# Performance work log

Measured on AMD Instinct MI355X. Metric: run time of the kernel, lower is better.

Reference implementation:

```python
import jax, jax.numpy as jnp
import numpy as np

SCALES = (8, 16, 32)
RATIOS = (0.5, 1.0, 2.0)
STRIDE = 16
K = len(SCALES) * len(RATIOS)
PRE_NMS = 6000
POST_NMS = 2000
NMS_THRESH = 0.7
ROIS_PER_IMG = 128
FG_ROIS = 32
FG_THRESH = 0.5
BG_HI = 0.5
BG_LO = 0.1
NUM_GT = 20
BBOX_CLIP = 4.135  # log(1000/16), standard delta clamp


def _generate_anchors(image_width, image_height):
    base = float(STRIDE)
    ctr = (base - 1.0) / 2.0
    size = base * base
    ratios = np.array(RATIOS, dtype=np.float64)
    scales = np.array(SCALES, dtype=np.float64)
    ws = np.round(np.sqrt(size / ratios))
    hs = np.round(ws * ratios)
    ws = (ws[:, None] * scales[None, :]).reshape(-1)  # (K,) ratio-major
    hs = (hs[:, None] * scales[None, :]).reshape(-1)
    anchors = np.stack([ctr - 0.5 * (ws - 1), ctr - 0.5 * (hs - 1),
                        ctr + 0.5 * (ws - 1), ctr + 0.5 * (hs - 1)], axis=1)  # (K,4)
    fw = image_width // STRIDE
    fh = image_height // STRIDE
    sx = np.arange(fw) * STRIDE
    sy = np.arange(fh) * STRIDE
    sxx, syy = np.meshgrid(sx, sy)  # (fh, fw)
    shifts = np.stack([sxx.ravel(), syy.ravel(), sxx.ravel(), syy.ravel()], axis=1)  # (fh*fw,4)
    all_anchors = (shifts[:, None, :] + anchors[None, :, :]).reshape(-1, 4)  # (fh*fw*K,4), K fastest
    return jnp.asarray(all_anchors, jnp.float32)


def _conv2d(x, w, b):
    y = jax.lax.conv_general_dilated(x, w, (1, 1), 'SAME',
                                     dimension_numbers=('NHWC', 'HWIO', 'NHWC'))
    return y + b


def _bbox_transform_inv(anchors, deltas):
    w = anchors[:, 2] - anchors[:, 0] + 1.0
    h = anchors[:, 3] - anchors[:, 1] + 1.0
    cx = anchors[:, 0] + 0.5 * w
    cy = anchors[:, 1] + 0.5 * h
    dx, dy = deltas[:, 0], deltas[:, 1]
    dw = jnp.clip(deltas[:, 2], -BBOX_CLIP, BBOX_CLIP)
    dh = jnp.clip(deltas[:, 3], -BBOX_CLIP, BBOX_CLIP)
    pcx = dx * w + cx
    pcy = dy * h + cy
    pw = jnp.exp(dw) * w
    ph = jnp.exp(dh) * h
    return jnp.stack([pcx - 0.5 * pw, pcy - 0.5 * ph,
                      pcx + 0.5 * pw, pcy + 0.5 * ph], axis=1)


def _pairwise_iou(a, b):
    area_a = (a[:, 2] - a[:, 0] + 1.0) * (a[:, 3] - a[:, 1] + 1.0)
    area_b = (b[:, 2] - b[:, 0] + 1.0) * (b[:, 3] - b[:, 1] + 1.0)
    xx1 = jnp.maximum(a[:, None, 0], b[None, :, 0])
    yy1 = jnp.maximum(a[:, None, 1], b[None, :, 1])
    xx2 = jnp.minimum(a[:, None, 2], b[None, :, 2])
    yy2 = jnp.minimum(a[:, None, 3], b[None, :, 3])
    iw = jnp.clip(xx2 - xx1 + 1.0, 0.0)
    ih = jnp.clip(yy2 - yy1 + 1.0, 0.0)
    inter = iw * ih
    return inter / (area_a[:, None] + area_b[None, :] - inter)


def _nms_keep(boxes, thresh):
    # boxes assumed sorted by score descending; greedy suppression
    n = boxes.shape[0]
    iou = _pairwise_iou(boxes, boxes)  # (n, n)
    idx = jnp.arange(n)
    def body(i, keep):
        sup = (iou[i] > thresh) & (idx > i)
        return jnp.where(keep[i], keep & ~sup, keep)
    return jax.lax.fori_loop(0, n, body, jnp.ones((n,), jnp.bool_))


def _forward(inputs, w_shared, b_shared, w_cls, b_cls, w_bbox, b_bbox,
             gt_boxes, image_width, image_height):
    fh = image_height // STRIDE
    fw = image_width // STRIDE
    anchors = _generate_anchors(image_width, image_height)  # (fh*fw*K, 4)

    shared = _conv2d(inputs, w_shared, b_shared)
    rpn_cls_score = _conv2d(shared, w_cls, b_cls)      # (1, fh, fw, 2K)
    rpn_bbox_pred = _conv2d(shared, w_bbox, b_bbox)    # (1, fh, fw, 4K)

    # softmax over the 2 (bg, fg) channels per anchor
    cls_prob = jax.nn.softmax(rpn_cls_score.reshape(1, fh, fw, K, 2), axis=-1)
    fg_scores = cls_prob[..., 1].reshape(-1)           # (fh*fw*K,)
    deltas = rpn_bbox_pred.reshape(-1, 4)              # (fh*fw*K, 4)

    # ---- proposal_layer ----
    proposals = _bbox_transform_inv(anchors, deltas)
    proposals = jnp.stack([
        jnp.clip(proposals[:, 0], 0.0, image_width - 1.0),
        jnp.clip(proposals[:, 1], 0.0, image_height - 1.0),
        jnp.clip(proposals[:, 2], 0.0, image_width - 1.0),
        jnp.clip(proposals[:, 3], 0.0, image_height - 1.0)], axis=1)

    top_scores, order = jax.lax.top_k(fg_scores, PRE_NMS)
    top_boxes = proposals[order]                       # (PRE_NMS, 4), score-sorted

    keep = _nms_keep(jax.lax.stop_gradient(top_boxes), NMS_THRESH)
    n = PRE_NMS
    rank = jnp.where(keep, jnp.arange(n), n + jnp.arange(n))
    sel = jnp.argsort(rank)[:POST_NMS]                 # kept boxes first, score order
    roi_boxes = top_boxes[sel]                         # (POST_NMS, 4)
    roi_scores = top_scores[sel]
    rois = jnp.concatenate([jnp.zeros((POST_NMS, 1), roi_boxes.dtype), roi_boxes], axis=1)

    # ---- proposal_target_layer (deterministic top-k sampling) ----
    ov = _pairwise_iou(roi_boxes, gt_boxes[:, :4])     # (POST_NMS, NUM_GT)
    max_ov = ov.max(axis=1)
    fg_key = jnp.where(max_ov >= FG_THRESH, max_ov, -1.0)
    _, fg_idx = jax.lax.top_k(fg_key, FG_ROIS)
    bg_key = jnp.where((max_ov < BG_HI) & (max_ov >= BG_LO), max_ov, -1.0)
    _, bg_idx = jax.lax.top_k(bg_key, ROIS_PER_IMG - FG_ROIS)
    keep_inds = jnp.concatenate([fg_idx, bg_idx])      # (128,)
    return rois[keep_inds]                             # (128, 5)


def setup_inputs() -> dict:
    key = jax.random.key(0)
    ks = jax.random.split(key, 10)
    C_in, C_mid = 1024, 256
    inputs = jax.random.normal(ks[0], (1, 64, 64, C_in), jnp.float32)
    w_shared = jax.random.normal(ks[1], (3, 3, C_in, C_mid), jnp.float32) * np.sqrt(2.0 / (9 * C_in))
    b_shared = jnp.zeros((C_mid,), jnp.float32)
    w_cls = jax.random.normal(ks[2], (1, 1, C_mid, 2 * K), jnp.float32) * np.sqrt(2.0 / C_mid)
    b_cls = jnp.zeros((2 * K,), jnp.float32)
    w_bbox = jax.random.normal(ks[3], (1, 1, C_mid, 4 * K), jnp.float32) * (0.1 * np.sqrt(2.0 / C_mid))
    b_bbox = jnp.zeros((4 * K,), jnp.float32)
    # valid gt boxes inside a 1024x1024 image
    cx = jax.random.uniform(ks[4], (NUM_GT,), minval=100.0, maxval=900.0)
    cy = jax.random.uniform(ks[5], (NUM_GT,), minval=100.0, maxval=900.0)
    bw = jax.random.uniform(ks[6], (NUM_GT,), minval=32.0, maxval=300.0)
    bh = jax.random.uniform(ks[7], (NUM_GT,), minval=32.0, maxval=300.0)
    cls = jax.random.randint(ks[8], (NUM_GT,), 1, 21).astype(jnp.float32)
    gt_boxes = jnp.stack([jnp.clip(cx - bw / 2, 0.0, 1023.0), jnp.clip(cy - bh / 2, 0.0, 1023.0),
                          jnp.clip(cx + bw / 2, 0.0, 1023.0), jnp.clip(cy + bh / 2, 0.0, 1023.0),
                          cls], axis=1)
    return {"inputs": inputs, "w_shared": w_shared, "b_shared": b_shared,
            "w_cls": w_cls, "b_cls": b_cls, "w_bbox": w_bbox, "b_bbox": b_bbox,
            "gt_boxes": gt_boxes, "image_width": 1024, "image_height": 1024}


def reference(inputs, w_shared, b_shared, w_cls, b_cls, w_bbox, b_bbox,
              gt_boxes, image_width, image_height):
    return _forward(inputs, w_shared, b_shared, w_cls, b_cls, w_bbox, b_bbox,
                    gt_boxes, image_width, image_height)
```

## Files before the change

### kernel.cpp

```cpp
#include <hip/hip_runtime.h>
#include <cstdint>
#include <cstddef>

#define M_POS 4096
#define NCH   256
#define KTOT  9216
#define NANCH 36864
#define NSORT 65536
#define PRE   6000
#define POST  2000
#define NGRP  94
#define MROW  6016
#define NSLOT 14

typedef unsigned long long u64;
typedef unsigned int u32;

__device__ __forceinline__ u32 ord_f32(float f) {
  u32 u = __float_as_uint(f);
  return (u & 0x80000000u) ? ~u : (u | 0x80000000u);
}

__global__ __launch_bounds__(256) void conv3x3(const float* __restrict__ in,
                                               const float* __restrict__ wgt,
                                               float* __restrict__ part,
                                               int kPer) {
  __shared__ __align__(16) float As[16][128];
  __shared__ __align__(16) float Bs[16][128];
  int tid = threadIdx.x;
  int bm = blockIdx.x << 7;
  int bn = blockIdx.y << 7;
  int kBeg = blockIdx.z * kPer;
  int am = tid & 127;
  int aq = (tid >> 7) << 2;
  int gm = bm + am;
  int y = gm >> 6, x = gm & 63;
  int bkk = tid >> 5;
  int bn4 = (tid & 31) << 2;
  int ty = tid >> 4, tx = tid & 15;

  float acc[8][8];
#pragma unroll
  for (int i = 0; i < 8; ++i)
#pragma unroll
    for (int j = 0; j < 8; ++j) acc[i][j] = 0.f;

  for (int k0 = kBeg; k0 < kBeg + kPer; k0 += 16) {
#pragma unroll
    for (int p = 0; p < 2; ++p) {
      int kk = aq + (p << 3);
      int k = k0 + kk;
      int tap = k >> 10;
      int c = k & 1023;
      int iy = y + tap / 3 - 1;
      int ix = x + tap % 3 - 1;
      float4 v = make_float4(0.f, 0.f, 0.f, 0.f);
      if (iy >= 0 && iy < 64 && ix >= 0 && ix < 64)
        v = *(const float4*)(in + (size_t)((((iy << 6) + ix) << 10) + c));
      As[kk + 0][am] = v.x;
      As[kk + 1][am] = v.y;
      As[kk + 2][am] = v.z;
      As[kk + 3][am] = v.w;
    }
#pragma unroll
    for (int p = 0; p < 2; ++p) {
      int kk = bkk + (p << 3);
      *(float4*)&Bs[kk][bn4] =
          *(const float4*)(wgt + (size_t)(k0 + kk) * NCH + bn + bn4);
    }
    __syncthreads();
#pragma unroll
    for (int kk = 0; kk < 16; ++kk) {
      float4 a0 = *(const float4*)&As[kk][ty << 2];
      float4 a1 = *(const float4*)&As[kk][64 + (ty << 2)];
      float4 b0 = *(const float4*)&Bs[kk][tx << 2];
      float4 b1 = *(const float4*)&Bs[kk][64 + (tx << 2)];
      float a[8] = {a0.x, a0.y, a0.z, a0.w, a1.x, a1.y, a1.z, a1.w};
      float b[8] = {b0.x, b0.y, b0.z, b0.w, b1.x, b1.y, b1.z, b1.w};
#pragma unroll
      for (int i = 0; i < 8; ++i)
#pragma unroll
        for (int j = 0; j < 8; ++j) acc[i][j] += a[i] * b[j];
    }
    __syncthreads();
  }
  size_t ob = (size_t)blockIdx.z * ((size_t)M_POS * NCH);
#pragma unroll
  for (int i = 0; i < 8; ++i) {
    int row = bm + ((i < 4) ? ((ty << 2) + i) : (64 + (ty << 2) + i - 4));
    float4 o0 = make_float4(acc[i][0], acc[i][1], acc[i][2], acc[i][3]);
    float4 o1 = make_float4(acc[i][4], acc[i][5], acc[i][6], acc[i][7]);
    *(float4*)(part + ob + (size_t)row * NCH + bn + (tx << 2)) = o0;
    *(float4*)(part + ob + (size_t)row * NCH + bn + 64 + (tx << 2)) = o1;
  }
}

__global__ __launch_bounds__(256) void reduce_bias(const float* __restrict__ part,
                                                   const float* __restrict__ bias,
                                                   float* __restrict__ outp, int ks) {
  int idx = blockIdx.x * 256 + threadIdx.x;
  float v = 0.f;
  for (int s = 0; s < ks; ++s) v += part[(size_t)s * (M_POS * NCH) + idx];
  outp[idx] = v + bias[idx & 255];
}

__global__ __launch_bounds__(64) void conv1x1(const float* __restrict__ sh,
                                              const float* __restrict__ wc,
                                              const float* __restrict__ bc,
                                              const float* __restrict__ wb,
                                              const float* __restrict__ bb2,
                                              float* __restrict__ cls,
                                              float* __restrict__ bbox) {
  __shared__ float row[256];
  int pos = blockIdx.x;
  int tid = threadIdx.x;
  *(float4*)&row[tid * 4] = *(const float4*)(sh + (size_t)pos * 256 + tid * 4);
  __syncthreads();
  if (tid < 18) {
    float acc = bc[tid];
    for (int c = 0; c < 256; ++c) acc += row[c] * wc[c * 18 + tid];
    cls[(size_t)pos * 18 + tid] = acc;
  } else if (tid < 54) {
    int n = tid - 18;
    float acc = bb2[n];
    for (int c = 0; c < 256; ++c) acc += row[c] * wb[c * 36 + n];
    bbox[(size_t)pos * 36 + n] = acc;
  }
}

__global__ __launch_bounds__(256) void proposals_k(const float* __restrict__ cls,
                                                   const float* __restrict__ bb,
                                                   float* __restrict__ scores,
                                                   float* __restrict__ prop) {
  int idx = blockIdx.x * 256 + threadIdx.x;
  if (idx >= NANCH) return;
  int a = idx % 9;
  int pos = idx / 9;
  int x = pos & 63, y = pos >> 6;
  float s0 = cls[(size_t)pos * 18 + 2 * a];
  float s1 = cls[(size_t)pos * 18 + 2 * a + 1];
  float mx = fmaxf(s0, s1);
  float e0 = expf(s0 - mx), e1 = expf(s1 - mx);
  scores[idx] = e1 / (e0 + e1);
  const float AW[9] = {184.f, 368.f, 736.f, 128.f, 256.f, 512.f, 88.f, 176.f, 352.f};
  const float AH[9] = {96.f, 192.f, 384.f, 128.f, 256.f, 512.f, 176.f, 352.f, 704.f};
  float w = AW[a], h = AH[a];
  float cx = (float)(x * 16) + 8.0f;
  float cy = (float)(y * 16) + 8.0f;
  float dx = bb[(size_t)pos * 36 + 4 * a + 0];
  float dy = bb[(size_t)pos * 36 + 4 * a + 1];
  float dw = bb[(size_t)pos * 36 + 4 * a + 2];
  float dh = bb[(size_t)pos * 36 + 4 * a + 3];
  dw = fminf(fmaxf(dw, -4.135f), 4.135f);
  dh = fminf(fmaxf(dh, -4.135f), 4.135f);
  float pcx = dx * w + cx;
  float pcy = dy * h + cy;
  float pw = expf(dw) * w;
  float ph = expf(dh) * h;
  float x1 = pcx - 0.5f * pw, y1 = pcy - 0.5f * ph;
  float x2 = pcx + 0.5f * pw, y2 = pcy + 0.5f * ph;
  x1 = fminf(fmaxf(x1, 0.f), 1023.f);
  y1 = fminf(fmaxf(y1, 0.f), 1023.f);
  x2 = fminf(fmaxf(x2, 0.f), 1023.f);
  y2 = fminf(fmaxf(y2, 0.f), 1023.f);
  prop[(size_t)idx * 4 + 0] = x1;
  prop[(size_t)idx * 4 + 1] = y1;
  prop[(size_t)idx * 4 + 2] = x2;
  prop[(size_t)idx * 4 + 3] = y2;
}

__global__ __launch_bounds__(256) void build_keys(const float* __restrict__ scores,
                                                  u64* __restrict__ keys) {
  int i = blockIdx.x * 256 + threadIdx.x;
  if (i >= NSORT) return;
  u64 k = 0ull;
  if (i < NANCH) {
    u32 u = ord_f32(scores[i]);
    k = ((u64)u << 32) | (u64)(0xFFFFFFFFu - (u32)i);
  }
  keys[i] = k;
}

__global__ __launch_bounds__(1024) void sort_local(u64* keys) {
  __shared__ u64 s[2048];
  int base = blockIdx.x * 2048;
  s[threadIdx.x] = keys[base + threadIdx.x];
  s[threadIdx.x + 1024] = keys[base + threadIdx.x + 1024];
  __syncthreads();
  for (int k = 2; k <= 2048; k <<= 1) {
    for (int j = k >> 1; j >= 1; j >>= 1) {
      int t = threadIdx.x;
      int i = ((t & ~(j - 1)) << 1) | (t & (j - 1));
      int p = i | j;
      bool desc = (((base + i) & k) == 0);
      u64 a = s[i], b = s[p];
      if (desc ? (a < b) : (a > b)) { s[i] = b; s[p] = a; }
      __syncthreads();
    }
  }
  keys[base + threadIdx.x] = s[threadIdx.x];
  keys[base + threadIdx.x + 1024] = s[threadIdx.x + 1024];
}

__device__ __forceinline__ void cmpswap(u64& a, u64& b, bool desc) {
  if (desc ? (a < b) : (a > b)) { u64 t = a; a = b; b = t; }
}

__global__ __launch_bounds__(256) void sort_gstep(u64* keys, int k, int j) {
  int t = blockIdx.x * 256 + threadIdx.x;
  int i = ((t & ~(j - 1)) << 1) | (t & (j - 1));
  int p = i | j;
  bool desc = ((i & k) == 0);
  u64 a = keys[i], b = keys[p];
  if (desc ? (a < b) : (a > b)) { keys[i] = b; keys[p] = a; }
}

__global__ __launch_bounds__(256) void sort_gstep2(u64* keys, int k, int j) {
  int t = blockIdx.x * 256 + threadIdx.x;
  int j2 = j >> 1;
  int a = ((t & ~(j2 - 1)) << 1) | (t & (j2 - 1));
  int i0 = ((a & ~(j - 1)) << 1) | (a & (j - 1));
  int i1 = i0 | j2, i2 = i0 | j, i3 = i0 | j | j2;
  bool desc = ((i0 & k) == 0);
  u64 v0 = keys[i0], v1 = keys[i1], v2 = keys[i2], v3 = keys[i3];
  cmpswap(v0, v2, desc);
  cmpswap(v1, v3, desc);
  cmpswap(v0, v1, desc);
  cmpswap(v2, v3, desc);
  keys[i0] = v0; keys[i1] = v1; keys[i2] = v2; keys[i3] = v3;
}

__global__ __launch_bounds__(1024) void sort_lstep(u64* keys, int k) {
  __shared__ u64 s[2048];
  int base = blockIdx.x * 2048;
  s[threadIdx.x] = keys[base + threadIdx.x];
  s[threadIdx.x + 1024] = keys[base + threadIdx.x + 1024];
  __syncthreads();
  for (int j = 1024; j >= 1; j >>= 1) {
    int t = threadIdx.x;
    int i = ((t & ~(j - 1)) << 1) | (t & (j - 1));
    int p = i | j;
    bool desc = (((base + i) & k) == 0);
    u64 a = s[i], b = s[p];
    if (desc ? (a < b) : (a > b)) { s[i] = b; s[p] = a; }
    __syncthreads();
  }
  keys[base + threadIdx.x] = s[threadIdx.x];
  keys[base + threadIdx.x + 1024] = s[threadIdx.x + 1024];
}

__global__ __launch_bounds__(256) void gather_top(const u64* __restrict__ keys,
                                                  const float4* __restrict__ prop,
                                                  float4* __restrict__ topbox) {
  int i = blockIdx.x * 256 + threadIdx.x;
  if (i >= PRE) return;
  u64 kk = keys[i];
  u32 idx = 0xFFFFFFFFu - (u32)(kk & 0xFFFFFFFFull);
  topbox[i] = prop[idx];
}

__global__ __launch_bounds__(64) void nms_mask(const float4* __restrict__ boxes,
                                               u64* __restrict__ maskT) {
  __shared__ float4 cb[64];
  int ci = blockIdx.x, ri = blockIdx.y;
  int t = threadIdx.x;
  int col = (ci << 6) + t;
  cb[t] = (col < PRE) ? boxes[col] : make_float4(0.f, 0.f, 0.f, 0.f);
  __syncthreads();
  int r = (ri << 6) + t;
  if (r >= PRE) return;
  float4 rb = boxes[r];
  float ra = (rb.z - rb.x + 1.f) * (rb.w - rb.y + 1.f);
  u64 bits = 0ull;
  for (int cc = 0; cc < 64; ++cc) {
    int j = (ci << 6) + cc;
    if (j > r && j < PRE) {
      float4 b = cb[cc];
      float ba = (b.z - b.x + 1.f) * (b.w - b.y + 1.f);
      float xx1 = fmaxf(rb.x, b.x), yy1 = fmaxf(rb.y, b.y);
      float xx2 = fminf(rb.z, b.z), yy2 = fminf(rb.w, b.w);
      float iw = fmaxf(xx2 - xx1 + 1.f, 0.f);
      float ih = fmaxf(yy2 - yy1 + 1.f, 0.f);
      float inter = iw * ih;
      float iou = inter / (ra + ba - inter);
      if (iou > 0.7f) bits |= (1ull << cc);
    }
  }
  maskT[(size_t)ci * MROW + r] = bits;
}

__global__ __launch_bounds__(512, 2) void nms_scan(const u64* __restrict__ maskT,
                                                   u64* __restrict__ keepw) {
  __shared__ u64 keepS;
  __shared__ u64 extS;
  __shared__ u32 exitS;
  const int tid = threadIdx.x;
  const int lane = tid & 63, wv = tid >> 6;

  u64 acc[NSLOT], v[NSLOT];
#pragma unroll
  for (int i = 0; i < NSLOT; ++i) { acc[i] = 0ull; v[i] = 0ull; }

  if (wv > 0) {
#pragma unroll
    for (int i = 0; i < NSLOT; ++i) {
      int gp = wv + 7 * i;
      if (gp < NGRP) v[i] = maskT[(size_t)gp * MROW + lane];
    }
  }
  u64 x = 0ull;
  if (wv == 0) x = maskT[lane];
  u32 keptTot = 0;

  for (int g = 0; g < NGRP; ++g) {
    if (wv == 0) {
      u64 cur = 0ull;
      if (g > 0) {
        u64 e = extS;
        u32 elo = __builtin_amdgcn_readfirstlane((u32)(e & 0xFFFFFFFFull));
        u32 ehi = __builtin_amdgcn_readfirstlane((u32)(e >> 32));
        cur = ((u64)ehi << 32) | (u64)elo;
      }
      u32 xlo = (u32)(x & 0xFFFFFFFFull);
      u32 xhi = (u32)(x >> 32);
      u64 keep = 0ull;
#pragma unroll
      for (int t = 0; t < 64; ++t) {
        u32 mlo = __builtin_amdgcn_readlane(xlo, t);
        u32 mhi = __builtin_amdgcn_readlane(xhi, t);
        u64 mt = ((u64)mhi << 32) | (u64)mlo;
        u64 sup = (cur >> t) & 1ull;
        u64 sel = sup - 1ull;
        keep |= (1ull << t) & sel;
        cur |= mt & sel;
      }
      if (g == NGRP - 1) keep &= (1ull << 48) - 1ull;
      keptTot += (u32)__popcll(keep);
      if (lane == 0) {
        keepS = keep;
        exitS = (keptTot >= POST) ? 1u : 0u;
        keepw[g] = keep;
      }
      if (g + 1 < NGRP) {
        int ii = ((g + 1) << 6) + lane;
        x = (ii < PRE) ? maskT[(size_t)(g + 1) * MROW + ii] : 0ull;
      }
    }
    asm volatile("s_waitcnt lgkmcnt(0)" ::: "memory");
    __builtin_amdgcn_sched_barrier(0);
    __builtin_amdgcn_s_barrier();
    __builtin_amdgcn_sched_barrier(0);
    u32 ex = exitS;
    u64 kb = keepS;
    if (ex) {
      for (int z = g + 1 + tid; z < NGRP; z += 512) keepw[z] = 0ull;
      return;
    }
    if (wv > 0) {
      u64 sel2 = ((kb >> lane) & 1ull) ? ~0ull : 0ull;
      u64 e = 0ull;
      bool own = false;
#pragma unroll
      for (int i = 0; i < NSLOT; ++i) {
        int gp = wv + 7 * i;
        if (gp < NGRP && gp > g) {
          acc[i] |= (v[i] & sel2);
          if (gp == g + 1) { e = acc[i]; own = true; }
        }
      }
      if (own) {
#pragma unroll
        for (int s = 1; s < 64; s <<= 1) e |= __shfl_xor(e, s, 64);
        if (lane == 0) extS = e;
      }
      int col = ((g + 1) << 6) + lane;
#pragma unroll
      for (int i = 0; i < NSLOT; ++i) {
        int gp = wv + 7 * i;
        if (gp < NGRP && gp > g + 1) v[i] = maskT[(size_t)gp * MROW + col];
      }
    }
    asm volatile("s_waitcnt lgkmcnt(0)" ::: "memory");
    __builtin_amdgcn_sched_barrier(0);
    __builtin_amdgcn_s_barrier();
    __builtin_amdgcn_sched_barrier(0);
  }
}

__global__ __launch_bounds__(1024) void select_rois(const u64* __restrict__ keepw,
                                                    const float4* __restrict__ topbox,
                                                    float4* __restrict__ roibox) {
  __shared__ u32 wscan[NGRP + 1];
  __shared__ u32 wc[NGRP];
  int tid = threadIdx.x;
  if (tid < NGRP) wc[tid] = (u32)__popcll(keepw[tid]);
  __syncthreads();
  if (tid == 0) {
    u32 r = 0;
    for (int g = 0; g < NGRP; ++g) { wscan[g] = r; r += wc[g]; }
    wscan[NGRP] = r;
  }
  __syncthreads();
  u32 ktot = wscan[NGRP];
  for (int i = tid; i < PRE; i += 1024) {
    int g = i >> 6, t = i & 63;
    u64 w = keepw[g];
    bool kept = (w >> t) & 1ull;
    u32 pk = wscan[g] + (u32)__popcll(w & ((1ull << t) - 1ull));
    u32 pos = kept ? pk : (ktot + (u32)i - pk);
    if (pos < POST) roibox[pos] = topbox[i];
  }
}

__device__ void bitonic2048_desc(u64* s) {
  int tid = threadIdx.x;
  for (int k = 2; k <= 2048; k <<= 1) {
    for (int j = k >> 1; j >= 1; j >>= 1) {
      int i = ((tid & ~(j - 1)) << 1) | (tid & (j - 1));
      int p = i | j;
      bool desc = ((i & k) == 0);
      u64 a = s[i], b = s[p];
      if (desc ? (a < b) : (a > b)) { s[i] = b; s[p] = a; }
      __syncthreads();
    }
  }
}

__global__ __launch_bounds__(1024) void roi_sample(const float4* __restrict__ roibox,
                                                   const float* __restrict__ gt,
                                                   float* __restrict__ out) {
  __shared__ float mov[POST];
  __shared__ u64 sk[2048];
  __shared__ float gtb[20][4];
  __shared__ int fgsel[32];
  __shared__ int bgsel[96];
  int tid = threadIdx.x;
  if (tid < 20) {
    gtb[tid][0] = gt[tid * 5 + 0];
    gtb[tid][1] = gt[tid * 5 + 1];
    gtb[tid][2] = gt[tid * 5 + 2];
    gtb[tid][3] = gt[tid * 5 + 3];
  }
  __syncthreads();
  for (int i = tid; i < POST; i += 1024) {
    float4 b = roibox[i];
    float aa = (b.z - b.x + 1.f) * (b.w - b.y + 1.f);
    float m = -3.402823466e38f;
    for (int t = 0; t < 20; ++t) {
      float gx1 = gtb[t][0], gy1 = gtb[t][1], gx2 = gtb[t][2], gy2 = gtb[t][3];
      float ga = (gx2 - gx1 + 1.f) * (gy2 - gy1 + 1.f);
      float xx1 = fmaxf(b.x, gx1), yy1 = fmaxf(b.y, gy1);
      float xx2 = fminf(b.z, gx2), yy2 = fminf(b.w, gy2);
      float iw = fmaxf(xx2 - xx1 + 1.f, 0.f);
      float ih = fmaxf(yy2 - yy1 + 1.f, 0.f);
      float inter = iw * ih;
      float iou = inter / (aa + ga - inter);
      m = fmaxf(m, iou);
    }
    mov[i] = m;
  }
  __syncthreads();
  for (int i = tid; i < 2048; i += 1024) {
    float key;
    if (i < POST) { float v = mov[i]; key = (v >= 0.5f) ? v : -1.0f; }
    else key = -2.0f;
    sk[i] = ((u64)ord_f32(key) << 32) | (u64)(2047u - (u32)i);
  }
  __syncthreads();
  bitonic2048_desc(sk);
  if (tid < 32) fgsel[tid] = (int)(2047u - (u32)(sk[tid] & 0xFFFFFFFFull));
  __syncthreads();
  for (int i = tid; i < 2048; i += 1024) {
    float key;
    if (i < POST) {
      float v = mov[i];
      key = (v < 0.5f && v >= 0.1f) ? v : -1.0f;
    } else key = -2.0f;
    sk[i] = ((u64)ord_f32(key) << 32) | (u64)(2047u - (u32)i);
  }
  __syncthreads();
  bitonic2048_desc(sk);
  if (tid < 96) bgsel[tid] = (int)(2047u - (u32)(sk[tid] & 0xFFFFFFFFull));
  __syncthreads();
  if (tid < 128) {
    int idx = (tid < 32) ? fgsel[tid] : bgsel[tid - 32];
    float4 b = roibox[idx];
    out[tid * 5 + 0] = 0.f;
    out[tid * 5 + 1] = b.x;
    out[tid * 5 + 2] = b.y;
    out[tid * 5 + 3] = b.z;
    out[tid * 5 + 4] = b.w;
  }
}

extern "C" void kernel_launch(void* const* d_in, const int* in_sizes, int n_in,
                              void* d_out, int out_size, void* d_ws, size_t ws_size,
                              hipStream_t stream) {
  const float* in   = (const float*)d_in[0];
  const float* wsh  = (const float*)d_in[1];
  const float* bsh  = (const float*)d_in[2];
  const float* wcls = (const float*)d_in[3];
  const float* bcls = (const float*)d_in[4];
  const float* wbb  = (const float*)d_in[5];
  const float* bbb  = (const float*)d_in[6];
  const float* gt   = (const float*)d_in[7];

  char* w = (char*)d_ws;
  const size_t OFF_SHARED = 0;
  const size_t OFF_CLS    = 4194304;
  const size_t OFF_BBOX   = 4489216;
  const size_t OFF_SCORES = 5079040;
  const size_t OFF_PROP   = 5226496;
  const size_t OFF_KEYS   = 0;
  const size_t OFF_TOPBOX = 524288;
  const size_t OFF_MASK   = 620288;
  const size_t OFF_KEEPW  = 5144320;
  const size_t OFF_ROIBOX = 5145088;
  const size_t OFF_PART   = 5816320;

  float* sharedb = (float*)(w + OFF_SHARED);
  float* cls     = (float*)(w + OFF_CLS);
  float* bbox    = (float*)(w + OFF_BBOX);
  float* scores  = (float*)(w + OFF_SCORES);
  float* prop    = (float*)(w + OFF_PROP);
  u64*   keys    = (u64*)(w + OFF_KEYS);
  float4* topbox = (float4*)(w + OFF_TOPBOX);
  u64*   maskT   = (u64*)(w + OFF_MASK);
  u64*   keepw   = (u64*)(w + OFF_KEEPW);
  float4* roibox = (float4*)(w + OFF_ROIBOX);
  float* out     = (float*)d_out;

  const size_t SLICE = (size_t)M_POS * NCH * 4;
  int KS = 1;
  if (ws_size >= OFF_PART + 8 * SLICE) KS = 8;
  else if (ws_size >= OFF_PART + 4 * SLICE) KS = 4;
  else if (ws_size >= OFF_PART + 2 * SLICE) KS = 2;
  float* part = (KS > 1) ? (float*)(w + OFF_PART) : sharedb;

  conv3x3<<<dim3(32, 2, KS), 256, 0, stream>>>(in, wsh, part, KTOT / KS);
  reduce_bias<<<4096, 256, 0, stream>>>(part, bsh, sharedb, KS);
  conv1x1<<<4096, 64, 0, stream>>>(sharedb, wcls, bcls, wbb, bbb, cls, bbox);
  proposals_k<<<144, 256, 0, stream>>>(cls, bbox, scores, prop);
  build_keys<<<256, 256, 0, stream>>>(scores, keys);
  sort_local<<<32, 1024, 0, stream>>>(keys);
  for (int k = 4096; k <= NSORT; k <<= 1) {
    int j = k >> 1;
    while (j >= 4096) {
      sort_gstep2<<<64, 256, 0, stream>>>(keys, k, j);
      j >>= 2;
    }
    if (j == 2048) {
      sort_gstep<<<128, 256, 0, stream>>>(keys, k, j);
      j >>= 1;
    }
    sort_lstep<<<32, 1024, 0, stream>>>(keys, k);
  }
  gather_top<<<24, 256, 0, stream>>>(keys, (const float4*)prop, topbox);
  nms_mask<<<dim3(NGRP, NGRP), 64, 0, stream>>>(topbox, maskT);
  nms_scan<<<1, 512, 0, stream>>>(maskT, keepw);
  select_rois<<<1, 1024, 0, stream>>>(keepw, topbox, roibox);
  roi_sample<<<1, 1024, 0, stream>>>(roibox, gt, out);
}
```

Measured before the change: 576.0 us.

## Narrow conv3x3 tiles, raise split-K, and use 4096-element shared-memory sort blocks

The 3x3 conv GEMM tile shrinks from 128x128 to 128x64 per block, with 4 column blocks instead of 2 and split-K raised to 16 when workspace allows, so many more workgroups run on the GPU. The bitonic sort now works on 4096-key chunks in shared memory and uses a hand-unrolled launch sequence, which cuts the number of global merge passes and kernel launches. The trade-offs are more partial-sum traffic in reduce_bias, lower arithmetic intensity per conv tile, and more LDS per sort block.

```diff
diff --git a/kernel.cpp b/kernel.cpp
--- a/kernel.cpp
+++ b/kernel.cpp
@@ -26,24 +26,24 @@
                                                float* __restrict__ part,
                                                int kPer) {
   __shared__ __align__(16) float As[16][128];
-  __shared__ __align__(16) float Bs[16][128];
+  __shared__ __align__(16) float Bs[16][64];
   int tid = threadIdx.x;
   int bm = blockIdx.x << 7;
-  int bn = blockIdx.y << 7;
+  int bn = blockIdx.y << 6;
   int kBeg = blockIdx.z * kPer;
   int am = tid & 127;
   int aq = (tid >> 7) << 2;
   int gm = bm + am;
   int y = gm >> 6, x = gm & 63;
-  int bkk = tid >> 5;
-  int bn4 = (tid & 31) << 2;
+  int bkk = tid >> 4;
+  int bn4 = (tid & 15) << 2;
   int ty = tid >> 4, tx = tid & 15;
 
-  float acc[8][8];
+  float acc[8][4];
 #pragma unroll
   for (int i = 0; i < 8; ++i)
 #pragma unroll
-    for (int j = 0; j < 8; ++j) acc[i][j] = 0.f;
+    for (int j = 0; j < 4; ++j) acc[i][j] = 0.f;
 
   for (int k0 = kBeg; k0 < kBeg + kPer; k0 += 16) {
 #pragma unroll
@@ -62,25 +62,20 @@
       As[kk + 2][am] = v.z;
       As[kk + 3][am] = v.w;
     }
-#pragma unroll
-    for (int p = 0; p < 2; ++p) {
-      int kk = bkk + (p << 3);
-      *(float4*)&Bs[kk][bn4] =
-          *(const float4*)(wgt + (size_t)(k0 + kk) * NCH + bn + bn4);
-    }
+    *(float4*)&Bs[bkk][bn4] =
+        *(const float4*)(wgt + (size_t)(k0 + bkk) * NCH + bn + bn4);
     __syncthreads();
 #pragma unroll
     for (int kk = 0; kk < 16; ++kk) {
       float4 a0 = *(const float4*)&As[kk][ty << 2];
       float4 a1 = *(const float4*)&As[kk][64 + (ty << 2)];
       float4 b0 = *(const float4*)&Bs[kk][tx << 2];
-      float4 b1 = *(const float4*)&Bs[kk][64 + (tx << 2)];
       float a[8] = {a0.x, a0.y, a0.z, a0.w, a1.x, a1.y, a1.z, a1.w};
-      float b[8] = {b0.x, b0.y, b0.z, b0.w, b1.x, b1.y, b1.z, b1.w};
+      float b[4] = {b0.x, b0.y, b0.z, b0.w};
 #pragma unroll
       for (int i = 0; i < 8; ++i)
 #pragma unroll
-        for (int j = 0; j < 8; ++j) acc[i][j] += a[i] * b[j];
+        for (int j = 0; j < 4; ++j) acc[i][j] += a[i] * b[j];
     }
     __syncthreads();
   }
@@ -88,10 +83,8 @@
 #pragma unroll
   for (int i = 0; i < 8; ++i) {
     int row = bm + ((i < 4) ? ((ty << 2) + i) : (64 + (ty << 2) + i - 4));
-    float4 o0 = make_float4(acc[i][0], acc[i][1], acc[i][2], acc[i][3]);
-    float4 o1 = make_float4(acc[i][4], acc[i][5], acc[i][6], acc[i][7]);
-    *(float4*)(part + ob + (size_t)row * NCH + bn + (tx << 2)) = o0;
-    *(float4*)(part + ob + (size_t)row * NCH + bn + 64 + (tx << 2)) = o1;
+    float4 o = make_float4(acc[i][0], acc[i][1], acc[i][2], acc[i][3]);
+    *(float4*)(part + ob + (size_t)row * NCH + bn + (tx << 2)) = o;
   }
 }
 
@@ -181,25 +174,46 @@
   keys[i] = k;
 }
 
-__global__ __launch_bounds__(1024) void sort_local(u64* keys) {
-  __shared__ u64 s[2048];
-  int base = blockIdx.x * 2048;
-  s[threadIdx.x] = keys[base + threadIdx.x];
-  s[threadIdx.x + 1024] = keys[base + threadIdx.x + 1024];
-  __syncthreads();
-  for (int k = 2; k <= 2048; k <<= 1) {
+__global__ __launch_bounds__(1024) void sort_local4(u64* keys) {
+  __shared__ u64 s[4096];
+  int base = blockIdx.x * 4096;
+  for (int i = threadIdx.x; i < 4096; i += 1024) s[i] = keys[base + i];
+  __syncthreads();
+  for (int k = 2; k <= 4096; k <<= 1) {
     for (int j = k >> 1; j >= 1; j >>= 1) {
-      int t = threadIdx.x;
+#pragma unroll
+      for (int q = 0; q < 2; ++q) {
+        int t = threadIdx.x + (q << 10);
+        int i = ((t & ~(j - 1)) << 1) | (t & (j - 1));
+        int p = i | j;
+        bool desc = (((base + i) & k) == 0);
+        u64 a = s[i], b = s[p];
+        if (desc ? (a < b) : (a > b)) { s[i] = b; s[p] = a; }
+      }
+      __syncthreads();
+    }
+  }
+  for (int i = threadIdx.x; i < 4096; i += 1024) keys[base + i] = s[i];
+}
+
+__global__ __launch_bounds__(1024) void sort_lstep4(u64* keys, int k) {
+  __shared__ u64 s[4096];
+  int base = blockIdx.x * 4096;
+  for (int i = threadIdx.x; i < 4096; i += 1024) s[i] = keys[base + i];
+  __syncthreads();
+  for (int j = 2048; j >= 1; j >>= 1) {
+#pragma unroll
+    for (int q = 0; q < 2; ++q) {
+      int t = threadIdx.x + (q << 10);
       int i = ((t & ~(j - 1)) << 1) | (t & (j - 1));
       int p = i | j;
       bool desc = (((base + i) & k) == 0);
       u64 a = s[i], b = s[p];
       if (desc ? (a < b) : (a > b)) { s[i] = b; s[p] = a; }
-      __syncthreads();
-    }
-  }
-  keys[base + threadIdx.x] = s[threadIdx.x];
-  keys[base + threadIdx.x + 1024] = s[threadIdx.x + 1024];
+    }
+    __syncthreads();
+  }
+  for (int i = threadIdx.x; i < 4096; i += 1024) keys[base + i] = s[i];
 }
 
 __device__ __forceinline__ void cmpswap(u64& a, u64& b, bool desc) {
@@ -228,25 +242,6 @@
   cmpswap(v0, v1, desc);
   cmpswap(v2, v3, desc);
   keys[i0] = v0; keys[i1] = v1; keys[i2] = v2; keys[i3] = v3;
-}
-
-__global__ __launch_bounds__(1024) void sort_lstep(u64* keys, int k) {
-  __shared__ u64 s[2048];
-  int base = blockIdx.x * 2048;
-  s[threadIdx.x] = keys[base + threadIdx.x];
-  s[threadIdx.x + 1024] = keys[base + threadIdx.x + 1024];
-  __syncthreads();
-  for (int j = 1024; j >= 1; j >>= 1) {
-    int t = threadIdx.x;
-    int i = ((t & ~(j - 1)) << 1) | (t & (j - 1));
-    int p = i | j;
-    bool desc = (((base + i) & k) == 0);
-    u64 a = s[i], b = s[p];
-    if (desc ? (a < b) : (a > b)) { s[i] = b; s[p] = a; }
-    __syncthreads();
-  }
-  keys[base + threadIdx.x] = s[threadIdx.x];
-  keys[base + threadIdx.x + 1024] = s[threadIdx.x + 1024];
 }
 
 __global__ __launch_bounds__(256) void gather_top(const u64* __restrict__ keys,
@@ -532,29 +527,29 @@
 
   const size_t SLICE = (size_t)M_POS * NCH * 4;
   int KS = 1;
-  if (ws_size >= OFF_PART + 8 * SLICE) KS = 8;
-  else if (ws_size >= OFF_PART + 4 * SLICE) KS = 4;
-  else if (ws_size >= OFF_PART + 2 * SLICE) KS = 2;
+  if      (ws_size >= OFF_PART + 16 * SLICE) KS = 16;
+  else if (ws_size >= OFF_PART + 8 * SLICE)  KS = 8;
+  else if (ws_size >= OFF_PART + 4 * SLICE)  KS = 4;
+  else if (ws_size >= OFF_PART + 2 * SLICE)  KS = 2;
   float* part = (KS > 1) ? (float*)(w + OFF_PART) : sharedb;
 
-  conv3x3<<<dim3(32, 2, KS), 256, 0, stream>>>(in, wsh, part, KTOT / KS);
+  conv3x3<<<dim3(32, 4, KS), 256, 0, stream>>>(in, wsh, part, KTOT / KS);
   reduce_bias<<<4096, 256, 0, stream>>>(part, bsh, sharedb, KS);
   conv1x1<<<4096, 64, 0, stream>>>(sharedb, wcls, bcls, wbb, bbb, cls, bbox);
   proposals_k<<<144, 256, 0, stream>>>(cls, bbox, scores, prop);
   build_keys<<<256, 256, 0, stream>>>(scores, keys);
-  sort_local<<<32, 1024, 0, stream>>>(keys);
-  for (int k = 4096; k <= NSORT; k <<= 1) {
-    int j = k >> 1;
-    while (j >= 4096) {
-      sort_gstep2<<<64, 256, 0, stream>>>(keys, k, j);
-      j >>= 2;
-    }
-    if (j == 2048) {
-      sort_gstep<<<128, 256, 0, stream>>>(keys, k, j);
-      j >>= 1;
-    }
-    sort_lstep<<<32, 1024, 0, stream>>>(keys, k);
-  }
+  sort_local4<<<16, 1024, 0, stream>>>(keys);
+  sort_gstep<<<128, 256, 0, stream>>>(keys, 8192, 4096);
+  sort_lstep4<<<16, 1024, 0, stream>>>(keys, 8192);
+  sort_gstep2<<<64, 256, 0, stream>>>(keys, 16384, 8192);
+  sort_lstep4<<<16, 1024, 0, stream>>>(keys, 16384);
+  sort_gstep2<<<64, 256, 0, stream>>>(keys, 32768, 16384);
+  sort_gstep<<<128, 256, 0, stream>>>(keys, 32768, 4096);
+  sort_lstep4<<<16, 1024, 0, stream>>>(keys, 32768);
+  sort_gstep2<<<64, 256, 0, stream>>>(keys, 65536, 32768);
+  sort_gstep2<<<64, 256, 0, stream>>>(keys, 65536, 8192);
+  sort_lstep4<<<16, 1024, 0, stream>>>(keys, 65536);
+
   gather_top<<<24, 256, 0, stream>>>(keys, (const float4*)prop, topbox);
   nms_mask<<<dim3(NGRP, NGRP), 64, 0, stream>>>(topbox, maskT);
   nms_scan<<<1, 512, 0, stream>>>(maskT, keepw);
```

Result: slower. 605.6 us (+5.1%).
